# Performance work log

Measured on AMD Instinct MI355X. Metric: run time of the kernel, lower is better.

The kernel has to match this reference:

```python
import jax, jax.numpy as jnp
import numpy as np

B, S, C = 16, 4096, 512   # genes, splice sites per gene, site rep channels
J = 4096                  # unique junctions per gene
T, K = 64, 32             # transcripts per gene, junctions per transcript
H = 1024                  # layer_channels; in_channels = 2*C = 1024
STD = 0.02                # config.initializer_range


def setup_inputs() -> dict:
    key = jax.random.key(0)
    ks = jax.random.split(key, 8)
    return {
        "splice_site_reps": jax.random.normal(ks[0], (B, S, C), jnp.float32),
        # indices in [0, S+2): values S -> gene_start token, S+1 -> gene_end token
        "don_idx": jax.random.randint(ks[1], (B, J), 0, S + 2, jnp.int32),
        "acc_idx": jax.random.randint(ks[2], (B, J), 0, S + 2, jnp.int32),
        "transcript_junctions": jax.random.randint(ks[3], (B, T, K), 0, J, jnp.int32),
        "W1": jax.random.normal(ks[4], (2 * C, H), jnp.float32) * STD,
        "b1": jnp.zeros((H,), jnp.float32),
        "W2": jax.random.normal(ks[5], (H, H), jnp.float32) * STD,
        "b2": jnp.zeros((H,), jnp.float32),
        "W3": jax.random.normal(ks[6], (H, 1), jnp.float32) * STD,
        "b3": jnp.zeros((1,), jnp.float32),
        "gene_start_rep": jnp.zeros((C,), jnp.float32),
        "gene_end_rep": jnp.zeros((C,), jnp.float32),
        "ref_potential": jnp.zeros((1,), jnp.float32),
    }


def reference(splice_site_reps, don_idx, acc_idx, transcript_junctions,
              W1, b1, W2, b2, W3, b3,
              gene_start_rep, gene_end_rep, ref_potential):
    b = splice_site_reps.shape[0]
    # augment per-gene site table with gene_start / gene_end reps -> [B, S+2, C]
    aug = jnp.concatenate([
        splice_site_reps,
        jnp.broadcast_to(gene_start_rep, (b, 1, C)),
        jnp.broadcast_to(gene_end_rep, (b, 1, C)),
    ], axis=1)
    don_emb = jnp.take_along_axis(aug, don_idx[:, :, None], axis=1)   # [B,J,C]
    acc_emb = jnp.take_along_axis(aug, acc_idx[:, :, None], axis=1)   # [B,J,C]
    x = jnp.concatenate([don_emb, acc_emb], axis=-1)                  # [B,J,2C]
    # SpliceosomeNet: Linear-ReLU-Linear-ReLU-Linear(->1)
    h = jax.nn.relu(x @ W1 + b1)
    h = jax.nn.relu(h @ W2 + b2)
    pot = (h @ W3 + b3)[..., 0]                                       # [B,J]
    # transcript total potential = sum of its junction potentials
    tj = transcript_junctions.reshape(b, T * K)
    tpot = jnp.take_along_axis(pot, tj, axis=1).reshape(b, T, K).sum(-1)  # [B,T]
    all_pot = jnp.concatenate([tpot, jnp.broadcast_to(ref_potential, (b, 1))], axis=1)
    return jax.nn.softmax(all_pot, axis=-1)                           # [B,T+1]
```

## Files before the change

kernel.cpp:

```cpp
#include <hip/hip_runtime.h>
#include <hip/hip_bf16.h>
#include <stdint.h>
#include <stddef.h>

#define NB 16
#define NS 4096
#define NSA 4098
#define NC 512
#define NJ 4096
#define NT 64
#define NKJ 32
#define KD 1024

#define NJC 2048
#define NMC (NB * NJC)

#define PREP_W_BLKS 2048
#define PREP_AUG_BLKS ((NB * NSA) / 4)
#define PREP_POT_BLKS 32

typedef __hip_bfloat16 bf16;
typedef __attribute__((ext_vector_type(8))) short bf16x8;
typedef __attribute__((ext_vector_type(4))) float f32x4;

#define BM 128
#define BN 128
#define BK 64

__device__ __forceinline__ void gload_lds16(const bf16* g, bf16* l) {
  __builtin_amdgcn_global_load_lds(
      (const __attribute__((address_space(1))) void*)g,
      (__attribute__((address_space(3))) void*)l, 16, 0, 0);
}

__device__ __forceinline__ void tile_from_bid(int bid, int& row0, int& col0) {
  const int row_idx = ((bid >> 6) << 3) | (bid & 7);
  const int col_idx = (bid >> 3) & 7;
  row0 = row_idx * BM;
  col0 = col_idx * BN;
}

__global__ __launch_bounds__(1024) void compact_kernel(
    const int* __restrict__ tj,
    int* __restrict__ rows_list,
    int* __restrict__ pmap) {
  const int b = blockIdx.x;
  const int tid = threadIdx.x;
  __shared__ unsigned char flg[NJ];
  __shared__ int psum[1024];
  *(uint32_t*)&flg[tid * 4] = 0u;
  __syncthreads();
#pragma unroll
  for (int k = 0; k < 2; k++) {
    const int j = tj[b * (NT * NKJ) + tid * 2 + k];
    flg[j] = 1;
  }
  __syncthreads();
  const int j0 = tid * 4;
  const int f0 = flg[j0], f1 = flg[j0 + 1], f2 = flg[j0 + 2], f3 = flg[j0 + 3];
  const int ls = f0 + f1 + f2 + f3;
  psum[tid] = ls;
  __syncthreads();
  for (int o = 1; o < 1024; o <<= 1) {
    const int v = (tid >= o) ? psum[tid - o] : 0;
    __syncthreads();
    psum[tid] += v;
    __syncthreads();
  }
  const int total = psum[1023];
  int p = psum[tid] - ls;
  if (f0) { rows_list[b * NJC + p] = j0;     pmap[b * NJ + j0]     = p; p++; }
  if (f1) { rows_list[b * NJC + p] = j0 + 1; pmap[b * NJ + j0 + 1] = p; p++; }
  if (f2) { rows_list[b * NJC + p] = j0 + 2; pmap[b * NJ + j0 + 2] = p; p++; }
  if (f3) { rows_list[b * NJC + p] = j0 + 3; pmap[b * NJ + j0 + 3] = p; p++; }
  for (int i = total + tid; i < NJC; i += 1024) rows_list[b * NJC + i] = 0;
}

__global__ void prep_kernel(const float* __restrict__ W1,
                            bf16* __restrict__ W1t,
                            const float* __restrict__ W2,
                            bf16* __restrict__ W2t,
                            const float* __restrict__ ssr,
                            const float* __restrict__ gstart,
                            const float* __restrict__ gend,
                            bf16* __restrict__ aug,
                            float* __restrict__ pot) {
  const int bid = blockIdx.x;
  const int tid = threadIdx.x;
  if (bid < PREP_W_BLKS) {
    __shared__ bf16 tile[32][33];
    const float* W = (bid >= 1024) ? W2 : W1;
    bf16* Wt = (bid >= 1024) ? W2t : W1t;
    const int pos = bid & 1023;
    const int n0 = (pos & 31) * 32;
    const int k0 = (pos >> 5) * 32;
    const int c = tid & 31;
    const int r0 = tid >> 5;
#pragma unroll
    for (int i = 0; i < 4; i++) {
      int r = r0 + i * 8;
      tile[r][c] = __float2bfloat16(W[(size_t)(k0 + r) * KD + (n0 + c)]);
    }
    __syncthreads();
#pragma unroll
    for (int i = 0; i < 4; i++) {
      int r = r0 + i * 8;
      Wt[(size_t)(n0 + r) * KD + (k0 + c)] = tile[c][r];
    }
  } else if (bid < PREP_W_BLKS + PREP_AUG_BLKS) {
    const int row = (bid - PREP_W_BLKS) * 4 + (tid >> 6);
    const int i = tid & 63;
    const int b = row / NSA;
    const int s = row - b * NSA;
    const float* src;
    if (s < NS)       src = ssr + ((size_t)b * NS + s) * NC;
    else if (s == NS) src = gstart;
    else              src = gend;
    f32x4 f0 = *(const f32x4*)(src + 4 * i);
    f32x4 f1 = *(const f32x4*)(src + 256 + 4 * i);
    bf16* dst = aug + (size_t)row * NC;
    union { uint64_t u; bf16 e[4]; } a, b4;
    a.e[0] = __float2bfloat16(f0.x); a.e[1] = __float2bfloat16(f0.y);
    a.e[2] = __float2bfloat16(f0.z); a.e[3] = __float2bfloat16(f0.w);
    b4.e[0] = __float2bfloat16(f1.x); b4.e[1] = __float2bfloat16(f1.y);
    b4.e[2] = __float2bfloat16(f1.z); b4.e[3] = __float2bfloat16(f1.w);
    *(uint64_t*)(dst + 4 * i) = a.u;
    *(uint64_t*)(dst + 256 + 4 * i) = b4.u;
  } else {
    const int i = (bid - (PREP_W_BLKS + PREP_AUG_BLKS)) * 1024 + tid * 4;
    *(f32x4*)(pot + i) = (f32x4){0.f, 0.f, 0.f, 0.f};
  }
}

__global__ __launch_bounds__(256, 2) void gemm1_gather_kernel(
    const bf16* __restrict__ aug, const int* __restrict__ don,
    const int* __restrict__ acc, const int* __restrict__ rows_list,
    const bf16* __restrict__ Bt, const float* __restrict__ bias,
    bf16* __restrict__ Cout) {
  __shared__ __align__(16) bf16 As[BM * BK];
  __shared__ __align__(16) bf16 Bs[BN * BK];
  const int tid = threadIdx.x;
  const int wave = tid >> 6;
  const int lane = tid & 63;
  int row0, col0;
  tile_from_bid(blockIdx.x, row0, col0);
  const int wm = wave & 1;
  const int wn = wave >> 1;
  const int q = lane >> 4;
  const int rr = lane & 15;

  int mm[4], gg[4];
#pragma unroll
  for (int i = 0; i < 4; i++) {
    int L = wave * 256 + i * 64 + lane;
    int m = L >> 3;
    int g = (L & 7) ^ (m & 7);
    mm[i] = m; gg[i] = g;
  }

  const bf16* dp[4];
  const bf16* ap[4];
#pragma unroll
  for (int i = 0; i < 4; i++) {
    const int r = row0 + mm[i];
    const int b = r >> 11;
    const int jid = rows_list[r];
    dp[i] = aug + ((size_t)b * NSA + don[b * NJ + jid]) * NC;
    ap[i] = aug + ((size_t)b * NSA + acc[b * NJ + jid]) * NC;
  }

  f32x4 acc4[4][4] = {};

  for (int kt = 0; kt < KD / BK; ++kt) {
    const int ko = (kt & 7) * BK;
#pragma unroll
    for (int i = 0; i < 4; i++) {
      const bf16* abase = (kt < 8) ? dp[i] : ap[i];
      gload_lds16(abase + ko + gg[i] * 8,
                  As + (size_t)(wave * 256 + i * 64) * 8);
      gload_lds16(Bt + ((size_t)(col0 + mm[i]) * KD + kt * BK + gg[i] * 8),
                  Bs + (size_t)(wave * 256 + i * 64) * 8);
    }
    __syncthreads();
#pragma unroll
    for (int kk = 0; kk < 2; ++kk) {
      bf16x8 afr[4], bfr[4];
      const int g = kk * 4 + q;
#pragma unroll
      for (int mt = 0; mt < 4; mt++) {
        int m = wm * 64 + mt * 16 + rr;
        afr[mt] = *(const bf16x8*)(As + (m * 8 + (g ^ (m & 7))) * 8);
      }
#pragma unroll
      for (int nt = 0; nt < 4; nt++) {
        int n = wn * 64 + nt * 16 + rr;
        bfr[nt] = *(const bf16x8*)(Bs + (n * 8 + (g ^ (n & 7))) * 8);
      }
#pragma unroll
      for (int mt = 0; mt < 4; mt++)
#pragma unroll
        for (int nt = 0; nt < 4; nt++)
          acc4[mt][nt] = __builtin_amdgcn_mfma_f32_16x16x32_bf16(
              afr[mt], bfr[nt], acc4[mt][nt], 0, 0, 0);
    }
    __syncthreads();
  }

#pragma unroll
  for (int nt = 0; nt < 4; nt++) {
    const int col = col0 + wn * 64 + nt * 16 + rr;
    const float bv = bias[col];
#pragma unroll
    for (int mt = 0; mt < 4; mt++) {
      const int rbase = row0 + wm * 64 + mt * 16 + q * 4;
#pragma unroll
      for (int rg = 0; rg < 4; rg++) {
        float v = fmaxf(acc4[mt][nt][rg] + bv, 0.f);
        Cout[(size_t)(rbase + rg) * KD + col] = __float2bfloat16(v);
      }
    }
  }
}

__global__ __launch_bounds__(256, 2) void gemm2_kernel(
    const bf16* __restrict__ A, const bf16* __restrict__ Bt,
    const float* __restrict__ bias, const float* __restrict__ w3,
    float* __restrict__ pot) {
  __shared__ __align__(16) bf16 As[BM * BK];
  __shared__ __align__(16) bf16 Bs[BN * BK];
  const int tid = threadIdx.x;
  const int wave = tid >> 6;
  const int lane = tid & 63;
  int row0, col0;
  tile_from_bid(blockIdx.x, row0, col0);
  const int wm = wave & 1;
  const int wn = wave >> 1;
  const int q = lane >> 4;
  const int rr = lane & 15;

  int mm[4], gg[4];
#pragma unroll
  for (int i = 0; i < 4; i++) {
    int L = wave * 256 + i * 64 + lane;
    int m = L >> 3;
    int g = (L & 7) ^ (m & 7);
    mm[i] = m; gg[i] = g;
  }

  f32x4 acc4[4][4] = {};

  for (int kt = 0; kt < KD / BK; ++kt) {
#pragma unroll
    for (int i = 0; i < 4; i++) {
      gload_lds16(A + ((size_t)(row0 + mm[i]) * KD + kt * BK + gg[i] * 8),
                  As + (size_t)(wave * 256 + i * 64) * 8);
      gload_lds16(Bt + ((size_t)(col0 + mm[i]) * KD + kt * BK + gg[i] * 8),
                  Bs + (size_t)(wave * 256 + i * 64) * 8);
    }
    __syncthreads();
#pragma unroll
    for (int kk = 0; kk < 2; ++kk) {
      bf16x8 afr[4], bfr[4];
      const int g = kk * 4 + q;
#pragma unroll
      for (int mt = 0; mt < 4; mt++) {
        int m = wm * 64 + mt * 16 + rr;
        afr[mt] = *(const bf16x8*)(As + (m * 8 + (g ^ (m & 7))) * 8);
      }
#pragma unroll
      for (int nt = 0; nt < 4; nt++) {
        int n = wn * 64 + nt * 16 + rr;
        bfr[nt] = *(const bf16x8*)(Bs + (n * 8 + (g ^ (n & 7))) * 8);
      }
#pragma unroll
      for (int mt = 0; mt < 4; mt++)
#pragma unroll
        for (int nt = 0; nt < 4; nt++)
          acc4[mt][nt] = __builtin_amdgcn_mfma_f32_16x16x32_bf16(
              afr[mt], bfr[nt], acc4[mt][nt], 0, 0, 0);
    }
    __syncthreads();
  }

  float bv[4], wv[4];
#pragma unroll
  for (int nt = 0; nt < 4; nt++) {
    const int col = col0 + wn * 64 + nt * 16 + rr;
    bv[nt] = bias[col];
    wv[nt] = w3[col];
  }
#pragma unroll
  for (int mt = 0; mt < 4; mt++) {
#pragma unroll
    for (int rg = 0; rg < 4; rg++) {
      float s = 0.f;
#pragma unroll
      for (int nt = 0; nt < 4; nt++)
        s += fmaxf(acc4[mt][nt][rg] + bv[nt], 0.f) * wv[nt];
      s += __shfl_xor(s, 1);
      s += __shfl_xor(s, 2);
      s += __shfl_xor(s, 4);
      s += __shfl_xor(s, 8);
      if (rr == 0) {
        int row = row0 + wm * 64 + mt * 16 + q * 4 + rg;
        atomicAdd(&pot[row], s);
      }
    }
  }
}

__global__ void transcript_softmax_kernel(const float* __restrict__ pot,
                                          const int* __restrict__ tj,
                                          const int* __restrict__ pmap,
                                          const float* __restrict__ b3,
                                          const float* __restrict__ refp,
                                          float* __restrict__ out) {
  const int b = blockIdx.x;
  const int t = threadIdx.x;
  const int* tjb = tj + ((size_t)b * NT + t) * NKJ;
  const int* pm = pmap + (size_t)b * NJ;
  const float* pb = pot + (size_t)b * NJC;
  float s = 0.f;
#pragma unroll
  for (int k = 0; k < NKJ; k++) s += pb[pm[tjb[k]]];
  s += (float)NKJ * b3[0];
  const float ref = refp[0];
  float m = fmaxf(s, ref);
#pragma unroll
  for (int o = 1; o < 64; o <<= 1) m = fmaxf(m, __shfl_xor(m, o));
  const float e = expf(s - m);
  float denom = e;
#pragma unroll
  for (int o = 1; o < 64; o <<= 1) denom += __shfl_xor(denom, o);
  const float eref = expf(ref - m);
  denom += eref;
  out[b * (NT + 1) + t] = e / denom;
  if (t == 0) out[b * (NT + 1) + NT] = eref / denom;
}

extern "C" void kernel_launch(void* const* d_in, const int* in_sizes, int n_in,
                              void* d_out, int out_size, void* d_ws,
                              size_t ws_size, hipStream_t stream) {
  const float* ssr    = (const float*)d_in[0];
  const int*   don    = (const int*)d_in[1];
  const int*   acc    = (const int*)d_in[2];
  const int*   tj     = (const int*)d_in[3];
  const float* W1     = (const float*)d_in[4];
  const float* b1     = (const float*)d_in[5];
  const float* W2     = (const float*)d_in[6];
  const float* b2     = (const float*)d_in[7];
  const float* W3     = (const float*)d_in[8];
  const float* b3     = (const float*)d_in[9];
  const float* gstart = (const float*)d_in[10];
  const float* gend   = (const float*)d_in[11];
  const float* refp   = (const float*)d_in[12];
  float* out = (float*)d_out;

  char* ws = (char*)d_ws;
  bf16* W1t = (bf16*)ws;                 ws += (size_t)KD * KD * 2;
  bf16* W2t = (bf16*)ws;                 ws += (size_t)KD * KD * 2;
  bf16* aug = (bf16*)ws;                 ws += (size_t)NB * NSA * NC * 2;
  bf16* H1  = (bf16*)ws;                 ws += (size_t)NMC * KD * 2;
  float* pot = (float*)ws;               ws += (size_t)NMC * 4;
  int* rows_list = (int*)ws;             ws += (size_t)NB * NJC * 4;
  int* pmap = (int*)ws;                  ws += (size_t)NB * NJ * 4;

  compact_kernel<<<NB, 1024, 0, stream>>>(tj, rows_list, pmap);

  prep_kernel<<<PREP_W_BLKS + PREP_AUG_BLKS + PREP_POT_BLKS, 256, 0, stream>>>(
      W1, W1t, W2, W2t, ssr, gstart, gend, aug, pot);

  gemm1_gather_kernel<<<NMC / BM * (KD / BN), 256, 0, stream>>>(
      aug, don, acc, rows_list, W1t, b1, H1);

  gemm2_kernel<<<NMC / BM * (KD / BN), 256, 0, stream>>>(H1, W2t, b2, W3, pot);

  transcript_softmax_kernel<<<NB, 64, 0, stream>>>(pot, tj, pmap, b3, refp, out);
}
```

Baseline: 367.2 us.

## Skip unused site rows and empty GEMM tiles using per-gene junction counts

The compaction kernel now records how many junctions each gene actually uses and marks which splice-site rows are referenced by those junctions. The prep kernel converts only the marked rows to bf16, and both GEMMs map row tiles onto packed per-gene tile ranges, exiting early for tiles beyond each gene's count. The block-wide prefix scan is replaced by a wave-shuffle scan plus per-wave totals. This trims conversion traffic and the GEMM work spent on padding rows, in exchange for extra scattered flag writes and a per-block tile lookup loop.

```diff
diff --git a/kernel.cpp b/kernel.cpp
--- a/kernel.cpp
+++ b/kernel.cpp
@@ -6,6 +6,7 @@
 #define NB 16
 #define NS 4096
 #define NSA 4098
+#define SFS 4104
 #define NC 512
 #define NJ 4096
 #define NT 64
@@ -33,47 +34,87 @@
       (__attribute__((address_space(3))) void*)l, 16, 0, 0);
 }
 
-__device__ __forceinline__ void tile_from_bid(int bid, int& row0, int& col0) {
-  const int row_idx = ((bid >> 6) << 3) | (bid & 7);
-  const int col_idx = (bid >> 3) & 7;
-  row0 = row_idx * BM;
-  col0 = col_idx * BN;
+__device__ __forceinline__ void tile_from_bid(int bid, int& row_idx,
+                                              int& col_idx) {
+  row_idx = ((bid >> 6) << 3) | (bid & 7);
+  col_idx = (bid >> 3) & 7;
+}
+
+__device__ __forceinline__ int map_tile(const int* __restrict__ cnt,
+                                        int row_tile, int& b_out) {
+  int at = 0;
+#pragma unroll
+  for (int b = 0; b < NB; b++) {
+    const int g = (cnt[b] + (BM - 1)) >> 7;
+    if (row_tile < at + g) { b_out = b; return row_tile - at; }
+    at += g;
+  }
+  b_out = -1;
+  return 0;
 }
 
 __global__ __launch_bounds__(1024) void compact_kernel(
     const int* __restrict__ tj,
+    const int* __restrict__ don,
+    const int* __restrict__ acc,
     int* __restrict__ rows_list,
-    int* __restrict__ pmap) {
+    int* __restrict__ pmap,
+    int* __restrict__ cnt,
+    unsigned char* __restrict__ sflag) {
   const int b = blockIdx.x;
   const int tid = threadIdx.x;
+  const int lane = tid & 63;
+  const int wv = tid >> 6;
   __shared__ unsigned char flg[NJ];
-  __shared__ int psum[1024];
+  __shared__ int wtot[16];
+
   *(uint32_t*)&flg[tid * 4] = 0u;
+  unsigned char* sf = sflag + (size_t)b * SFS;
+  ((uint32_t*)sf)[tid] = 0u;
+  if (tid < SFS / 4 - 1024) ((uint32_t*)sf)[1024 + tid] = 0u;
   __syncthreads();
+
 #pragma unroll
   for (int k = 0; k < 2; k++) {
     const int j = tj[b * (NT * NKJ) + tid * 2 + k];
     flg[j] = 1;
   }
+  if (tid == 0) flg[0] = 1;
   __syncthreads();
+
   const int j0 = tid * 4;
   const int f0 = flg[j0], f1 = flg[j0 + 1], f2 = flg[j0 + 2], f3 = flg[j0 + 3];
   const int ls = f0 + f1 + f2 + f3;
-  psum[tid] = ls;
+
+  int x = ls;
+#pragma unroll
+  for (int o = 1; o < 64; o <<= 1) {
+    const int y = __shfl_up(x, o);
+    if (lane >= o) x += y;
+  }
+  if (lane == 63) wtot[wv] = x;
   __syncthreads();
-  for (int o = 1; o < 1024; o <<= 1) {
-    const int v = (tid >= o) ? psum[tid - o] : 0;
-    __syncthreads();
-    psum[tid] += v;
-    __syncthreads();
-  }
-  const int total = psum[1023];
-  int p = psum[tid] - ls;
-  if (f0) { rows_list[b * NJC + p] = j0;     pmap[b * NJ + j0]     = p; p++; }
-  if (f1) { rows_list[b * NJC + p] = j0 + 1; pmap[b * NJ + j0 + 1] = p; p++; }
-  if (f2) { rows_list[b * NJC + p] = j0 + 2; pmap[b * NJ + j0 + 2] = p; p++; }
-  if (f3) { rows_list[b * NJC + p] = j0 + 3; pmap[b * NJ + j0 + 3] = p; p++; }
-  for (int i = total + tid; i < NJC; i += 1024) rows_list[b * NJC + i] = 0;
+
+  int woff = 0, total = 0;
+#pragma unroll
+  for (int w = 0; w < 16; w++) {
+    const int t = wtot[w];
+    if (w < wv) woff += t;
+    total += t;
+  }
+  int p = woff + x - ls;
+
+  const int* donb = don + (size_t)b * NJ;
+  const int* accb = acc + (size_t)b * NJ;
+  int* rl = rows_list + (size_t)b * NJC;
+  int* pm = pmap + (size_t)b * NJ;
+  if (f0) { rl[p] = j0;     pm[j0]     = p; sf[donb[j0]]     = 1; sf[accb[j0]]     = 1; p++; }
+  if (f1) { rl[p] = j0 + 1; pm[j0 + 1] = p; sf[donb[j0 + 1]] = 1; sf[accb[j0 + 1]] = 1; p++; }
+  if (f2) { rl[p] = j0 + 2; pm[j0 + 2] = p; sf[donb[j0 + 2]] = 1; sf[accb[j0 + 2]] = 1; p++; }
+  if (f3) { rl[p] = j0 + 3; pm[j0 + 3] = p; sf[donb[j0 + 3]] = 1; sf[accb[j0 + 3]] = 1; p++; }
+
+  for (int i = total + tid; i < NJC; i += 1024) rl[i] = 0;
+  if (tid == 0) cnt[b] = total;
 }
 
 __global__ void prep_kernel(const float* __restrict__ W1,
@@ -83,6 +124,7 @@
                             const float* __restrict__ ssr,
                             const float* __restrict__ gstart,
                             const float* __restrict__ gend,
+                            const unsigned char* __restrict__ sflag,
                             bf16* __restrict__ aug,
                             float* __restrict__ pot) {
   const int bid = blockIdx.x;
@@ -112,6 +154,7 @@
     const int i = tid & 63;
     const int b = row / NSA;
     const int s = row - b * NSA;
+    if (!sflag[(size_t)b * SFS + s]) return;
     const float* src;
     if (s < NS)       src = ssr + ((size_t)b * NS + s) * NC;
     else if (s == NS) src = gstart;
@@ -135,15 +178,20 @@
 __global__ __launch_bounds__(256, 2) void gemm1_gather_kernel(
     const bf16* __restrict__ aug, const int* __restrict__ don,
     const int* __restrict__ acc, const int* __restrict__ rows_list,
-    const bf16* __restrict__ Bt, const float* __restrict__ bias,
-    bf16* __restrict__ Cout) {
+    const int* __restrict__ cnt, const bf16* __restrict__ Bt,
+    const float* __restrict__ bias, bf16* __restrict__ Cout) {
   __shared__ __align__(16) bf16 As[BM * BK];
   __shared__ __align__(16) bf16 Bs[BN * BK];
   const int tid = threadIdx.x;
   const int wave = tid >> 6;
   const int lane = tid & 63;
-  int row0, col0;
-  tile_from_bid(blockIdx.x, row0, col0);
+  int row_idx, col_idx;
+  tile_from_bid(blockIdx.x, row_idx, col_idx);
+  int gb;
+  const int lt = map_tile(cnt, row_idx, gb);
+  if (gb < 0) return;
+  const int grow0 = gb * NJC + lt * BM;
+  const int col0 = col_idx * BN;
   const int wm = wave & 1;
   const int wn = wave >> 1;
   const int q = lane >> 4;
@@ -162,11 +210,9 @@
   const bf16* ap[4];
 #pragma unroll
   for (int i = 0; i < 4; i++) {
-    const int r = row0 + mm[i];
-    const int b = r >> 11;
-    const int jid = rows_list[r];
-    dp[i] = aug + ((size_t)b * NSA + don[b * NJ + jid]) * NC;
-    ap[i] = aug + ((size_t)b * NSA + acc[b * NJ + jid]) * NC;
+    const int jid = rows_list[grow0 + mm[i]];
+    dp[i] = aug + ((size_t)gb * NSA + don[gb * NJ + jid]) * NC;
+    ap[i] = aug + ((size_t)gb * NSA + acc[gb * NJ + jid]) * NC;
   }
 
   f32x4 acc4[4][4] = {};
@@ -212,7 +258,7 @@
     const float bv = bias[col];
 #pragma unroll
     for (int mt = 0; mt < 4; mt++) {
-      const int rbase = row0 + wm * 64 + mt * 16 + q * 4;
+      const int rbase = grow0 + wm * 64 + mt * 16 + q * 4;
 #pragma unroll
       for (int rg = 0; rg < 4; rg++) {
         float v = fmaxf(acc4[mt][nt][rg] + bv, 0.f);
@@ -223,16 +269,21 @@
 }
 
 __global__ __launch_bounds__(256, 2) void gemm2_kernel(
-    const bf16* __restrict__ A, const bf16* __restrict__ Bt,
-    const float* __restrict__ bias, const float* __restrict__ w3,
-    float* __restrict__ pot) {
+    const bf16* __restrict__ A, const int* __restrict__ cnt,
+    const bf16* __restrict__ Bt, const float* __restrict__ bias,
+    const float* __restrict__ w3, float* __restrict__ pot) {
   __shared__ __align__(16) bf16 As[BM * BK];
   __shared__ __align__(16) bf16 Bs[BN * BK];
   const int tid = threadIdx.x;
   const int wave = tid >> 6;
   const int lane = tid & 63;
-  int row0, col0;
-  tile_from_bid(blockIdx.x, row0, col0);
+  int row_idx, col_idx;
+  tile_from_bid(blockIdx.x, row_idx, col_idx);
+  int gb;
+  const int lt = map_tile(cnt, row_idx, gb);
+  if (gb < 0) return;
+  const int grow0 = gb * NJC + lt * BM;
+  const int col0 = col_idx * BN;
   const int wm = wave & 1;
   const int wn = wave >> 1;
   const int q = lane >> 4;
@@ -252,7 +303,7 @@
   for (int kt = 0; kt < KD / BK; ++kt) {
 #pragma unroll
     for (int i = 0; i < 4; i++) {
-      gload_lds16(A + ((size_t)(row0 + mm[i]) * KD + kt * BK + gg[i] * 8),
+      gload_lds16(A + ((size_t)(grow0 + mm[i]) * KD + kt * BK + gg[i] * 8),
                   As + (size_t)(wave * 256 + i * 64) * 8);
       gload_lds16(Bt + ((size_t)(col0 + mm[i]) * KD + kt * BK + gg[i] * 8),
                   Bs + (size_t)(wave * 256 + i * 64) * 8);
@@ -302,7 +353,7 @@
       s += __shfl_xor(s, 4);
       s += __shfl_xor(s, 8);
       if (rr == 0) {
-        int row = row0 + wm * 64 + mt * 16 + q * 4 + rg;
+        int row = grow0 + wm * 64 + mt * 16 + q * 4 + rg;
         atomicAdd(&pot[row], s);
       }
     }
@@ -364,16 +415,21 @@
   float* pot = (float*)ws;               ws += (size_t)NMC * 4;
   int* rows_list = (int*)ws;             ws += (size_t)NB * NJC * 4;
   int* pmap = (int*)ws;                  ws += (size_t)NB * NJ * 4;
-
-  compact_kernel<<<NB, 1024, 0, stream>>>(tj, rows_list, pmap);
+  int* cnt = (int*)ws;                   ws += 64;
+  unsigned char* sflag = (unsigned char*)ws;  ws += (size_t)NB * SFS;
+
+  compact_kernel<<<NB, 1024, 0, stream>>>(tj, don, acc, rows_list, pmap, cnt,
+                                          sflag);
 
   prep_kernel<<<PREP_W_BLKS + PREP_AUG_BLKS + PREP_POT_BLKS, 256, 0, stream>>>(
-      W1, W1t, W2, W2t, ssr, gstart, gend, aug, pot);
-
-  gemm1_gather_kernel<<<NMC / BM * (KD / BN), 256, 0, stream>>>(
-      aug, don, acc, rows_list, W1t, b1, H1);
-
-  gemm2_kernel<<<NMC / BM * (KD / BN), 256, 0, stream>>>(H1, W2t, b2, W3, pot);
-
-  transcript_softmax_kernel<<<NB, 64, 0, stream>>>(pot, tj, pmap, b3, refp, out);
-}
+      W1, W1t, W2, W2t, ssr, gstart, gend, sflag, aug, pot);
+
+  gemm1_gather_kernel<<<(NMC / BM) * (KD / BN), 256, 0, stream>>>(
+      aug, don, acc, rows_list, cnt, W1t, b1, H1);
+
+  gemm2_kernel<<<(NMC / BM) * (KD / BN), 256, 0, stream>>>(H1, cnt, W2t, b2,
+                                                           W3, pot);
+
+  transcript_softmax_kernel<<<NB, 64, 0, stream>>>(pot, tj, pmap, b3, refp,
+                                                   out);
+}
```

After: 329.6 us, median of 2. 1.11x faster.
